# Performance work log

Measured on AMD Instinct MI355X. Metric: run time of the kernel, lower is better.

The kernel has to match this reference:

```python
import jax, jax.numpy as jnp
import numpy as np

DIM = 512
HEADS = 8
WINDOW = 128


def setup_inputs() -> dict:
    key = jax.random.key(0)
    k1, k2, k3, k4 = jax.random.split(key, 4)
    x = jax.random.normal(k1, (16, 4096, DIM), dtype=jnp.float32)
    w_qkv = jax.random.normal(k2, (3 * DIM, DIM), dtype=jnp.float32) * 0.02
    w_proj = jax.random.normal(k3, (DIM, DIM), dtype=jnp.float32) * 0.02
    b_proj = jax.random.normal(k4, (DIM,), dtype=jnp.float32) * 0.02
    return {"x": x, "w_qkv": w_qkv, "w_proj": w_proj, "b_proj": b_proj}


def reference(x, w_qkv, w_proj, b_proj):
    B0, T0, C = x.shape
    H = HEADS
    hd = C // H
    scale = hd ** (-0.5)
    W = WINDOW
    # split into independent windows: [B*T/W, W, C]
    xw = x.reshape(-1, W, C)
    Bw = xw.shape[0]
    # qkv projection (no bias), reshape to [3, Bw, H, W, hd]
    qkv = (xw @ w_qkv.T).reshape(Bw, W, 3, H, hd).transpose(2, 0, 3, 1, 4)
    q, k, v = qkv[0], qkv[1], qkv[2]
    # scaled scores per window: [Bw, H, W, W]
    attn = jnp.einsum("bhqd,bhkd->bhqk", q, k) * scale
    causal_mask = jnp.tril(jnp.ones((W, W), dtype=bool))
    attn = jnp.where(causal_mask, attn, -jnp.inf)
    attn = jax.nn.softmax(attn, axis=-1)
    out = jnp.einsum("bhqk,bhkd->bhqd", attn, v)  # [Bw, H, W, hd]
    out = out.transpose(0, 2, 1, 3).reshape(Bw, W, C)
    out = out @ w_proj.T + b_proj
    return out.reshape(B0, T0, C)
```

## Files before the change

kernel.cpp:

```cpp
#include <hip/hip_runtime.h>
#include <stdint.h>


typedef unsigned short ushort_t;
typedef __attribute__((ext_vector_type(8))) short short8;
typedef __attribute__((ext_vector_type(4))) float f32x4;
typedef __attribute__((ext_vector_type(4))) float f4v;
typedef __attribute__((ext_vector_type(4))) unsigned short us4;

static __device__ __forceinline__ unsigned short f2bf(float f) {
  unsigned int u = __float_as_uint(f);
  u += 0x7FFFu + ((u >> 16) & 1u);
  return (unsigned short)(u >> 16);
}

static __device__ __forceinline__ void gl_lds16(const ushort_t* g, ushort_t* l) {
  __builtin_amdgcn_global_load_lds(
      (const __attribute__((address_space(1))) void*)g,
      (__attribute__((address_space(3))) void*)l, 16, 0, 0);
}

__global__ __launch_bounds__(256) void cast_f32_bf16(const float* __restrict__ in,
                                                     ushort_t* __restrict__ out, int n4) {
  int i = blockIdx.x * 256 + threadIdx.x;
  if (i >= n4) return;
  f4v v = ((const f4v*)in)[i];
  us4 o;
  o.x = f2bf(v.x); o.y = f2bf(v.y); o.z = f2bf(v.z); o.w = f2bf(v.w);
  ((us4*)out)[i] = o;
}

__global__ __launch_bounds__(256) void qkv_gemm(const ushort_t* __restrict__ A,
                                                const ushort_t* __restrict__ B,
                                                ushort_t* __restrict__ qk,
                                                ushort_t* __restrict__ vT) {
  __shared__ __align__(16) ushort_t As[128 * 64];
  __shared__ __align__(16) ushort_t Bs[128 * 64];
  const int tid = threadIdx.x;
  const int lane = tid & 63;
  const int wv = tid >> 6;
  const int wr = wv >> 1, wc = wv & 1;
  const int m0 = blockIdx.x << 7;
  const int n0 = blockIdx.y << 7;
  const int lr = lane & 15;
  const int lg = lane >> 4;
  const int sw = lr & 7;

  f32x4 acc[4][4] = {};

  const int grow = tid >> 3;
  const int gcol = (((tid & 7) ^ (grow & 7)) << 3);
  const ushort_t* gA = A + (size_t)(m0 + grow) * 512 + gcol;
  const ushort_t* gB = B + (size_t)(n0 + grow) * 512 + gcol;

  for (int kk = 0; kk < 512; kk += 64) {
#pragma unroll
    for (int r = 0; r < 4; ++r) {
      gl_lds16(gA + (size_t)(r * 32) * 512 + kk, As + (size_t)(r * 256 + wv * 64) * 8);
      gl_lds16(gB + (size_t)(r * 32) * 512 + kk, Bs + (size_t)(r * 256 + wv * 64) * 8);
    }
    __syncthreads();
#pragma unroll
    for (int ks = 0; ks < 2; ++ks) {
      const int co = ((((ks << 2) | lg) ^ sw) << 3);
      short8 a[4], b[4];
#pragma unroll
      for (int mi = 0; mi < 4; ++mi)
        a[mi] = *(const short8*)(As + (wr * 64 + mi * 16 + lr) * 64 + co);
#pragma unroll
      for (int ni = 0; ni < 4; ++ni)
        b[ni] = *(const short8*)(Bs + (wc * 64 + ni * 16 + lr) * 64 + co);
#pragma unroll
      for (int mi = 0; mi < 4; ++mi)
#pragma unroll
        for (int ni = 0; ni < 4; ++ni)
          acc[mi][ni] = __builtin_amdgcn_mfma_f32_16x16x32_bf16(a[mi], b[ni], acc[mi][ni], 0, 0, 0);
    }
    __syncthreads();
  }

  const int lg4 = lg << 2;
  if (n0 < 1024) {
#pragma unroll
    for (int mi = 0; mi < 4; ++mi) {
      const int rbase = m0 + wr * 64 + mi * 16 + lg4;
#pragma unroll
      for (int ni = 0; ni < 4; ++ni) {
        const int col = n0 + wc * 64 + ni * 16 + lr;
#pragma unroll
        for (int rg = 0; rg < 4; ++rg)
          qk[(size_t)(rbase + rg) * 1024 + col] = f2bf(acc[mi][ni][rg]);
      }
    }
  } else {
    const int win = blockIdx.x;
#pragma unroll
    for (int mi = 0; mi < 4; ++mi) {
      const int t0 = wr * 64 + mi * 16 + lg4;
#pragma unroll
      for (int ni = 0; ni < 4; ++ni) {
        const int c = n0 - 1024 + wc * 64 + ni * 16 + lr;
        const int h = c >> 6, d = c & 63;
        us4 o;
        o.x = f2bf(acc[mi][ni][0]); o.y = f2bf(acc[mi][ni][1]);
        o.z = f2bf(acc[mi][ni][2]); o.w = f2bf(acc[mi][ni][3]);
        *(us4*)(vT + (size_t)((win * 8 + h) * 64 + d) * 128 + t0) = o;
      }
    }
  }
}

__global__ __launch_bounds__(256) void attn_kernel(const ushort_t* __restrict__ qk,
                                                   const ushort_t* __restrict__ vT,
                                                   ushort_t* __restrict__ attn_out) {
  __shared__ __align__(16) ushort_t smem[24576];
  ushort_t* qs = smem;
  ushort_t* ks_ = smem + 8192;
  ushort_t* vs = smem + 16384;
  ushort_t* ps = smem;

  const int tid = threadIdx.x;
  const int lane = tid & 63;
  const int wv = tid >> 6;
  const int win = blockIdx.x >> 3;
  const int h = blockIdx.x & 7;
  const int lr = lane & 15;
  const int lg = lane >> 4;
  const int lg4 = lg << 2;
  const int sw = lr & 7;

  const size_t qbase = (size_t)win * 128 * 1024 + h * 64;
#pragma unroll
  for (int r = 0; r < 4; ++r) {
    const int g = r * 256 + tid;
    const int t = g >> 3, ch = g & 7;
    short8 vq = *(const short8*)(qk + qbase + (size_t)t * 1024 + ch * 8);
    short8 vk = *(const short8*)(qk + qbase + 512 + (size_t)t * 1024 + ch * 8);
    const int st = t * 64 + ((ch ^ (t & 7)) << 3);
    *(short8*)(qs + st) = vq;
    *(short8*)(ks_ + st) = vk;
  }
  const size_t vbase = (size_t)(win * 8 + h) * 64 * 128;
#pragma unroll
  for (int r = 0; r < 4; ++r) {
    const int g = r * 256 + tid;
    const int d = g >> 4, ch = g & 15;
    short8 vvv = *(const short8*)(vT + vbase + (size_t)d * 128 + ch * 8);
    *(short8*)(vs + d * 128 + ((ch ^ (d & 7)) << 3)) = vvv;
  }
  __syncthreads();

  const int rt[2] = {wv, 7 - wv};

  f32x4 sacc[2][8] = {};
#pragma unroll
  for (int ks2 = 0; ks2 < 2; ++ks2) {
    const int co = ((((ks2 << 2) | lg) ^ sw) << 3);
    short8 a0 = *(const short8*)(qs + (rt[0] * 16 + lr) * 64 + co);
    short8 a1 = *(const short8*)(qs + (rt[1] * 16 + lr) * 64 + co);
#pragma unroll
    for (int ni = 0; ni < 8; ++ni) {
      if (ni <= rt[1]) {
        short8 b = *(const short8*)(ks_ + (ni * 16 + lr) * 64 + co);
        if (ni <= rt[0])
          sacc[0][ni] = __builtin_amdgcn_mfma_f32_16x16x32_bf16(a0, b, sacc[0][ni], 0, 0, 0);
        sacc[1][ni] = __builtin_amdgcn_mfma_f32_16x16x32_bf16(a1, b, sacc[1][ni], 0, 0, 0);
      }
    }
  }

  __syncthreads();

  const float C = 0.125f * 1.44269504f;
#pragma unroll
  for (int mi = 0; mi < 2; ++mi) {
    const int r = rt[mi];
    const int rb = r * 16;
#pragma unroll
    for (int ni = 0; ni < 8; ++ni) {
      if (ni <= r) {
#pragma unroll
        for (int rg = 0; rg < 4; ++rg) {
          const int row = rb + lg4 + rg;
          const int col = ni * 16 + lr;
          float e = __builtin_exp2f(sacc[mi][ni][rg] * C);
          e = (col <= row) ? e : 0.0f;
          ps[row * 128 + ((((col >> 3) ^ (row & 7)) << 3) | (col & 7))] = f2bf(e);
        }
      }
    }
    if (!(r & 1)) {
      const int col = (r + 1) * 16 + lr;
#pragma unroll
      for (int rg = 0; rg < 4; ++rg) {
        const int row = rb + lg4 + rg;
        ps[row * 128 + ((((col >> 3) ^ (row & 7)) << 3) | (col & 7))] = 0;
      }
    }
  }

  const short one_bf = (short)0x3F80;
  short8 ones;
#pragma unroll
  for (int j = 0; j < 8; ++j) ones[j] = (lr == 0) ? one_bf : (short)0;

  f32x4 oacc[2][4] = {};
  f32x4 sm[2] = {};
#pragma unroll
  for (int ks2 = 0; ks2 < 4; ++ks2) {
    const int co = ((((ks2 << 2) | lg) ^ sw) << 3);
    if (ks2 <= (rt[1] >> 1)) {
      short8 b[4];
#pragma unroll
      for (int nd = 0; nd < 4; ++nd)
        b[nd] = *(const short8*)(vs + (nd * 16 + lr) * 128 + co);
      short8 a1 = *(const short8*)(ps + (rt[1] * 16 + lr) * 128 + co);
#pragma unroll
      for (int nd = 0; nd < 4; ++nd)
        oacc[1][nd] = __builtin_amdgcn_mfma_f32_16x16x32_bf16(a1, b[nd], oacc[1][nd], 0, 0, 0);
      sm[1] = __builtin_amdgcn_mfma_f32_16x16x32_bf16(a1, ones, sm[1], 0, 0, 0);
      if (ks2 <= (rt[0] >> 1)) {
        short8 a0 = *(const short8*)(ps + (rt[0] * 16 + lr) * 128 + co);
#pragma unroll
        for (int nd = 0; nd < 4; ++nd)
          oacc[0][nd] = __builtin_amdgcn_mfma_f32_16x16x32_bf16(a0, b[nd], oacc[0][nd], 0, 0, 0);
        sm[0] = __builtin_amdgcn_mfma_f32_16x16x32_bf16(a0, ones, sm[0], 0, 0, 0);
      }
    }
  }

  const int src = lane & 48;
  const size_t obase = (size_t)win * 128 * 512 + h * 64;
#pragma unroll
  for (int mi = 0; mi < 2; ++mi) {
    const int rb = rt[mi] * 16;
    float rsv[4];
#pragma unroll
    for (int rg = 0; rg < 4; ++rg)
      rsv[rg] = 1.0f / __shfl(sm[mi][rg], src);
#pragma unroll
    for (int nd = 0; nd < 4; ++nd)
#pragma unroll
      for (int rg = 0; rg < 4; ++rg) {
        const int row = rb + lg4 + rg;
        const int col = nd * 16 + lr;
        attn_out[obase + (size_t)row * 512 + col] = f2bf(oacc[mi][nd][rg] * rsv[rg]);
      }
  }
}

__global__ __launch_bounds__(256) void proj_gemm(const ushort_t* __restrict__ A,
                                                 const ushort_t* __restrict__ B,
                                                 const float* __restrict__ bias,
                                                 float* __restrict__ out) {
  __shared__ __align__(16) ushort_t As[128 * 64];
  __shared__ __align__(16) ushort_t Bs[128 * 64];
  const int tid = threadIdx.x;
  const int lane = tid & 63;
  const int wv = tid >> 6;
  const int wr = wv >> 1, wc = wv & 1;
  const int m0 = blockIdx.x << 7;
  const int n0 = blockIdx.y << 7;
  const int lr = lane & 15;
  const int lg = lane >> 4;
  const int sw = lr & 7;

  f32x4 acc[4][4] = {};

  const int grow = tid >> 3;
  const int gcol = (((tid & 7) ^ (grow & 7)) << 3);
  const ushort_t* gA = A + (size_t)(m0 + grow) * 512 + gcol;
  const ushort_t* gB = B + (size_t)(n0 + grow) * 512 + gcol;

  for (int kk = 0; kk < 512; kk += 64) {
#pragma unroll
    for (int r = 0; r < 4; ++r) {
      gl_lds16(gA + (size_t)(r * 32) * 512 + kk, As + (size_t)(r * 256 + wv * 64) * 8);
      gl_lds16(gB + (size_t)(r * 32) * 512 + kk, Bs + (size_t)(r * 256 + wv * 64) * 8);
    }
    __syncthreads();
#pragma unroll
    for (int ks = 0; ks < 2; ++ks) {
      const int co = ((((ks << 2) | lg) ^ sw) << 3);
      short8 a[4], b[4];
#pragma unroll
      for (int mi = 0; mi < 4; ++mi)
        a[mi] = *(const short8*)(As + (wr * 64 + mi * 16 + lr) * 64 + co);
#pragma unroll
      for (int ni = 0; ni < 4; ++ni)
        b[ni] = *(const short8*)(Bs + (wc * 64 + ni * 16 + lr) * 64 + co);
#pragma unroll
      for (int mi = 0; mi < 4; ++mi)
#pragma unroll
        for (int ni = 0; ni < 4; ++ni)
          acc[mi][ni] = __builtin_amdgcn_mfma_f32_16x16x32_bf16(a[mi], b[ni], acc[mi][ni], 0, 0, 0);
    }
    __syncthreads();
  }

  const int lg4 = lg << 2;
#pragma unroll
  for (int mi = 0; mi < 4; ++mi) {
    const int rbase = m0 + wr * 64 + mi * 16 + lg4;
#pragma unroll
    for (int ni = 0; ni < 4; ++ni) {
      const int col = n0 + wc * 64 + ni * 16 + lr;
      const float bv = bias[col];
#pragma unroll
      for (int rg = 0; rg < 4; ++rg)
        out[(size_t)(rbase + rg) * 512 + col] = acc[mi][ni][rg] + bv;
    }
  }
}

extern "C" void kernel_launch(void* const* d_in, const int* in_sizes, int n_in,
                              void* d_out, int out_size, void* d_ws, size_t ws_size,
                              hipStream_t stream) {
  const float* x      = (const float*)d_in[0];
  const float* w_qkv  = (const float*)d_in[1];
  const float* w_proj = (const float*)d_in[2];
  const float* b_proj = (const float*)d_in[3];
  float* out = (float*)d_out;

  char* ws = (char*)d_ws;
  ushort_t* x_bf     = (ushort_t*)(ws);
  ushort_t* qk_ws    = (ushort_t*)(ws + 67108864);
  ushort_t* vT_ws    = (ushort_t*)(ws + 67108864 + 134217728);
  ushort_t* attn_ws  = (ushort_t*)(ws + 67108864 + 134217728 + 67108864);
  ushort_t* wqkv_bf  = (ushort_t*)(ws + 335544320);
  ushort_t* wproj_bf = (ushort_t*)(ws + 337117184);

  cast_f32_bf16<<<32768, 256, 0, stream>>>(x, x_bf, 8388608);
  cast_f32_bf16<<<768, 256, 0, stream>>>(w_qkv, wqkv_bf, 196608);
  cast_f32_bf16<<<256, 256, 0, stream>>>(w_proj, wproj_bf, 65536);

  qkv_gemm<<<dim3(512, 12), 256, 0, stream>>>(x_bf, wqkv_bf, qk_ws, vT_ws);
  attn_kernel<<<4096, 256, 0, stream>>>(qk_ws, vT_ws, attn_ws);
  proj_gemm<<<dim3(512, 4), 256, 0, stream>>>(attn_ws, wproj_bf, b_proj, out);
}
```

Baseline: 520.2 us.

## Triple-buffer GEMM K-loop with async LDS loads, 256x128 tiles and XCD remap

Result: faster. 477.0 us (-8.3%).

```diff
diff --git a/kernel.cpp b/kernel.cpp
--- a/kernel.cpp
+++ b/kernel.cpp
@@ -30,53 +30,80 @@
   ((us4*)out)[i] = o;
 }
 
-__global__ __launch_bounds__(256) void qkv_gemm(const ushort_t* __restrict__ A,
-                                                const ushort_t* __restrict__ B,
-                                                ushort_t* __restrict__ qk,
-                                                ushort_t* __restrict__ vT) {
-  __shared__ __align__(16) ushort_t As[128 * 64];
-  __shared__ __align__(16) ushort_t Bs[128 * 64];
+__global__ __launch_bounds__(512, 2) void qkv_gemm(const ushort_t* __restrict__ A,
+                                                   const ushort_t* __restrict__ B,
+                                                   ushort_t* __restrict__ qk,
+                                                   ushort_t* __restrict__ vT) {
+  __shared__ __align__(16) ushort_t smem[3 * 24576];
   const int tid = threadIdx.x;
   const int lane = tid & 63;
   const int wv = tid >> 6;
   const int wr = wv >> 1, wc = wv & 1;
-  const int m0 = blockIdx.x << 7;
-  const int n0 = blockIdx.y << 7;
   const int lr = lane & 15;
   const int lg = lane >> 4;
-  const int sw = lr & 7;
+
+  const int bid = blockIdx.x;
+  const int wg = (bid & 7) * 384 + (bid >> 3);
+  const int nb = wg % 12;
+  const int mb = wg / 12;
+  const int m0 = mb << 8;
+  const int n0 = nb << 7;
+
+  const int srow = tid >> 3;
+  const int ssw  = (((tid & 7) ^ (srow & 7)) << 3);
+  const ushort_t* gA = A + (size_t)(m0 + srow) * 512 + ssw;
+  const ushort_t* gB = B + (size_t)(n0 + srow) * 512 + ssw;
 
   f32x4 acc[4][4] = {};
 
-  const int grow = tid >> 3;
-  const int gcol = (((tid & 7) ^ (grow & 7)) << 3);
-  const ushort_t* gA = A + (size_t)(m0 + grow) * 512 + gcol;
-  const ushort_t* gB = B + (size_t)(n0 + grow) * 512 + gcol;
-
-  for (int kk = 0; kk < 512; kk += 64) {
-#pragma unroll
-    for (int r = 0; r < 4; ++r) {
-      gl_lds16(gA + (size_t)(r * 32) * 512 + kk, As + (size_t)(r * 256 + wv * 64) * 8);
-      gl_lds16(gB + (size_t)(r * 32) * 512 + kk, Bs + (size_t)(r * 256 + wv * 64) * 8);
-    }
-    __syncthreads();
+  auto STAGE = [&](int t, int q) {
+    ushort_t* Ab = smem + q * 24576;
+    ushort_t* Bb = Ab + 16384;
+    const int kk = t << 6;
+#pragma unroll
+    for (int r = 0; r < 4; ++r)
+      gl_lds16(gA + (size_t)(r * 64) * 512 + kk, Ab + (r * 512 + wv * 64) * 8);
+#pragma unroll
+    for (int r = 0; r < 2; ++r)
+      gl_lds16(gB + (size_t)(r * 64) * 512 + kk, Bb + (r * 512 + wv * 64) * 8);
+  };
+
+  STAGE(0, 0);
+  STAGE(1, 1);
+  asm volatile("s_waitcnt vmcnt(6)" ::: "memory");
+  __builtin_amdgcn_s_barrier();
+
+#pragma unroll
+  for (int t = 0; t < 8; ++t) {
+    const ushort_t* Ab = smem + (t % 3) * 24576;
+    const ushort_t* Bb = Ab + 16384;
+    short8 a[4][2], b[4][2];
 #pragma unroll
     for (int ks = 0; ks < 2; ++ks) {
-      const int co = ((((ks << 2) | lg) ^ sw) << 3);
-      short8 a[4], b[4];
+      const int co = ((((ks << 2) | lg) ^ (lr & 7)) << 3);
 #pragma unroll
       for (int mi = 0; mi < 4; ++mi)
-        a[mi] = *(const short8*)(As + (wr * 64 + mi * 16 + lr) * 64 + co);
+        a[mi][ks] = *(const short8*)(Ab + (wr * 64 + mi * 16 + lr) * 64 + co);
 #pragma unroll
       for (int ni = 0; ni < 4; ++ni)
-        b[ni] = *(const short8*)(Bs + (wc * 64 + ni * 16 + lr) * 64 + co);
+        b[ni][ks] = *(const short8*)(Bb + (wc * 64 + ni * 16 + lr) * 64 + co);
+    }
+    if (t + 2 < 8) STAGE(t + 2, (t + 2) % 3);
+    if (t < 7) {
+      if (t + 2 < 8) asm volatile("s_waitcnt vmcnt(6)" ::: "memory");
+      else           asm volatile("s_waitcnt vmcnt(0)" ::: "memory");
+      asm volatile("s_waitcnt lgkmcnt(0)" ::: "memory");
+      __builtin_amdgcn_s_barrier();
+    }
+    __builtin_amdgcn_s_setprio(1);
+#pragma unroll
+    for (int ks = 0; ks < 2; ++ks)
 #pragma unroll
       for (int mi = 0; mi < 4; ++mi)
 #pragma unroll
         for (int ni = 0; ni < 4; ++ni)
-          acc[mi][ni] = __builtin_amdgcn_mfma_f32_16x16x32_bf16(a[mi], b[ni], acc[mi][ni], 0, 0, 0);
-    }
-    __syncthreads();
+          acc[mi][ni] = __builtin_amdgcn_mfma_f32_16x16x32_bf16(a[mi][ks], b[ni][ks], acc[mi][ni], 0, 0, 0);
+    __builtin_amdgcn_s_setprio(0);
   }
 
   const int lg4 = lg << 2;
@@ -93,10 +120,11 @@
       }
     }
   } else {
-    const int win = blockIdx.x;
+    const int winb = (m0 >> 7) + (wr >> 1);
+    const int t0b = (wr & 1) * 64;
 #pragma unroll
     for (int mi = 0; mi < 4; ++mi) {
-      const int t0 = wr * 64 + mi * 16 + lg4;
+      const int t0 = t0b + mi * 16 + lg4;
 #pragma unroll
       for (int ni = 0; ni < 4; ++ni) {
         const int c = n0 - 1024 + wc * 64 + ni * 16 + lr;
@@ -104,7 +132,7 @@
         us4 o;
         o.x = f2bf(acc[mi][ni][0]); o.y = f2bf(acc[mi][ni][1]);
         o.z = f2bf(acc[mi][ni][2]); o.w = f2bf(acc[mi][ni][3]);
-        *(us4*)(vT + (size_t)((win * 8 + h) * 64 + d) * 128 + t0) = o;
+        *(us4*)(vT + (size_t)((winb * 8 + h) * 64 + d) * 128 + t0) = o;
       }
     }
   }
@@ -249,53 +277,80 @@
   }
 }
 
-__global__ __launch_bounds__(256) void proj_gemm(const ushort_t* __restrict__ A,
-                                                 const ushort_t* __restrict__ B,
-                                                 const float* __restrict__ bias,
-                                                 float* __restrict__ out) {
-  __shared__ __align__(16) ushort_t As[128 * 64];
-  __shared__ __align__(16) ushort_t Bs[128 * 64];
+__global__ __launch_bounds__(512, 2) void proj_gemm(const ushort_t* __restrict__ A,
+                                                    const ushort_t* __restrict__ B,
+                                                    const float* __restrict__ bias,
+                                                    float* __restrict__ out) {
+  __shared__ __align__(16) ushort_t smem[3 * 24576];
   const int tid = threadIdx.x;
   const int lane = tid & 63;
   const int wv = tid >> 6;
   const int wr = wv >> 1, wc = wv & 1;
-  const int m0 = blockIdx.x << 7;
-  const int n0 = blockIdx.y << 7;
   const int lr = lane & 15;
   const int lg = lane >> 4;
-  const int sw = lr & 7;
+
+  const int bid = blockIdx.x;
+  const int wg = (bid & 7) * 128 + (bid >> 3);
+  const int nb = wg & 3;
+  const int mb = wg >> 2;
+  const int m0 = mb << 8;
+  const int n0 = nb << 7;
+
+  const int srow = tid >> 3;
+  const int ssw  = (((tid & 7) ^ (srow & 7)) << 3);
+  const ushort_t* gA = A + (size_t)(m0 + srow) * 512 + ssw;
+  const ushort_t* gB = B + (size_t)(n0 + srow) * 512 + ssw;
 
   f32x4 acc[4][4] = {};
 
-  const int grow = tid >> 3;
-  const int gcol = (((tid & 7) ^ (grow & 7)) << 3);
-  const ushort_t* gA = A + (size_t)(m0 + grow) * 512 + gcol;
-  const ushort_t* gB = B + (size_t)(n0 + grow) * 512 + gcol;
-
-  for (int kk = 0; kk < 512; kk += 64) {
-#pragma unroll
-    for (int r = 0; r < 4; ++r) {
-      gl_lds16(gA + (size_t)(r * 32) * 512 + kk, As + (size_t)(r * 256 + wv * 64) * 8);
-      gl_lds16(gB + (size_t)(r * 32) * 512 + kk, Bs + (size_t)(r * 256 + wv * 64) * 8);
-    }
-    __syncthreads();
+  auto STAGE = [&](int t, int q) {
+    ushort_t* Ab = smem + q * 24576;
+    ushort_t* Bb = Ab + 16384;
+    const int kk = t << 6;
+#pragma unroll
+    for (int r = 0; r < 4; ++r)
+      gl_lds16(gA + (size_t)(r * 64) * 512 + kk, Ab + (r * 512 + wv * 64) * 8);
+#pragma unroll
+    for (int r = 0; r < 2; ++r)
+      gl_lds16(gB + (size_t)(r * 64) * 512 + kk, Bb + (r * 512 + wv * 64) * 8);
+  };
+
+  STAGE(0, 0);
+  STAGE(1, 1);
+  asm volatile("s_waitcnt vmcnt(6)" ::: "memory");
+  __builtin_amdgcn_s_barrier();
+
+#pragma unroll
+  for (int t = 0; t < 8; ++t) {
+    const ushort_t* Ab = smem + (t % 3) * 24576;
+    const ushort_t* Bb = Ab + 16384;
+    short8 a[4][2], b[4][2];
 #pragma unroll
     for (int ks = 0; ks < 2; ++ks) {
-      const int co = ((((ks << 2) | lg) ^ sw) << 3);
-      short8 a[4], b[4];
+      const int co = ((((ks << 2) | lg) ^ (lr & 7)) << 3);
 #pragma unroll
       for (int mi = 0; mi < 4; ++mi)
-        a[mi] = *(const short8*)(As + (wr * 64 + mi * 16 + lr) * 64 + co);
+        a[mi][ks] = *(const short8*)(Ab + (wr * 64 + mi * 16 + lr) * 64 + co);
 #pragma unroll
       for (int ni = 0; ni < 4; ++ni)
-        b[ni] = *(const short8*)(Bs + (wc * 64 + ni * 16 + lr) * 64 + co);
+        b[ni][ks] = *(const short8*)(Bb + (wc * 64 + ni * 16 + lr) * 64 + co);
+    }
+    if (t + 2 < 8) STAGE(t + 2, (t + 2) % 3);
+    if (t < 7) {
+      if (t + 2 < 8) asm volatile("s_waitcnt vmcnt(6)" ::: "memory");
+      else           asm volatile("s_waitcnt vmcnt(0)" ::: "memory");
+      asm volatile("s_waitcnt lgkmcnt(0)" ::: "memory");
+      __builtin_amdgcn_s_barrier();
+    }
+    __builtin_amdgcn_s_setprio(1);
+#pragma unroll
+    for (int ks = 0; ks < 2; ++ks)
 #pragma unroll
       for (int mi = 0; mi < 4; ++mi)
 #pragma unroll
         for (int ni = 0; ni < 4; ++ni)
-          acc[mi][ni] = __builtin_amdgcn_mfma_f32_16x16x32_bf16(a[mi], b[ni], acc[mi][ni], 0, 0, 0);
-    }
-    __syncthreads();
+          acc[mi][ni] = __builtin_amdgcn_mfma_f32_16x16x32_bf16(a[mi][ks], b[ni][ks], acc[mi][ni], 0, 0, 0);
+    __builtin_amdgcn_s_setprio(0);
   }
 
   const int lg4 = lg << 2;
@@ -334,7 +389,7 @@
   cast_f32_bf16<<<768, 256, 0, stream>>>(w_qkv, wqkv_bf, 196608);
   cast_f32_bf16<<<256, 256, 0, stream>>>(w_proj, wproj_bf, 65536);
 
-  qkv_gemm<<<dim3(512, 12), 256, 0, stream>>>(x_bf, wqkv_bf, qk_ws, vT_ws);
+  qkv_gemm<<<3072, 512, 0, stream>>>(x_bf, wqkv_bf, qk_ws, vT_ws);
   attn_kernel<<<4096, 256, 0, stream>>>(qk_ws, vT_ws, attn_ws);
-  proj_gemm<<<dim3(512, 4), 256, 0, stream>>>(attn_ws, wproj_bf, b_proj, out);
-}
+  proj_gemm<<<1024, 512, 0, stream>>>(attn_ws, wproj_bf, b_proj, out);
+}
```

## Use 256x256 tiles with 4-stage LDS pipeline and XCD-aware block mapping in GEMMs

Applied to the files above, without the earlier changes.

After: 492.1 us. 5.4% less time.

```diff
diff --git a/kernel.cpp b/kernel.cpp
--- a/kernel.cpp
+++ b/kernel.cpp
@@ -30,60 +30,78 @@
   ((us4*)out)[i] = o;
 }
 
-__global__ __launch_bounds__(256) void qkv_gemm(const ushort_t* __restrict__ A,
-                                                const ushort_t* __restrict__ B,
-                                                ushort_t* __restrict__ qk,
-                                                ushort_t* __restrict__ vT) {
-  __shared__ __align__(16) ushort_t As[128 * 64];
-  __shared__ __align__(16) ushort_t Bs[128 * 64];
+__global__ __launch_bounds__(512, 1) void qkv_gemm(const ushort_t* __restrict__ A,
+                                                   const ushort_t* __restrict__ B,
+                                                   ushort_t* __restrict__ qk,
+                                                   ushort_t* __restrict__ vT) {
+  __shared__ __align__(16) ushort_t smem[4 * 16384];
   const int tid = threadIdx.x;
   const int lane = tid & 63;
   const int wv = tid >> 6;
-  const int wr = wv >> 1, wc = wv & 1;
-  const int m0 = blockIdx.x << 7;
-  const int n0 = blockIdx.y << 7;
+  const int wr = wv >> 2;
+  const int wc = wv & 3;
   const int lr = lane & 15;
   const int lg = lane >> 4;
-  const int sw = lr & 7;
-
-  f32x4 acc[4][4] = {};
-
-  const int grow = tid >> 3;
-  const int gcol = (((tid & 7) ^ (grow & 7)) << 3);
-  const ushort_t* gA = A + (size_t)(m0 + grow) * 512 + gcol;
-  const ushort_t* gB = B + (size_t)(n0 + grow) * 512 + gcol;
-
-  for (int kk = 0; kk < 512; kk += 64) {
-#pragma unroll
-    for (int r = 0; r < 4; ++r) {
-      gl_lds16(gA + (size_t)(r * 32) * 512 + kk, As + (size_t)(r * 256 + wv * 64) * 8);
-      gl_lds16(gB + (size_t)(r * 32) * 512 + kk, Bs + (size_t)(r * 256 + wv * 64) * 8);
-    }
-    __syncthreads();
-#pragma unroll
-    for (int ks = 0; ks < 2; ++ks) {
-      const int co = ((((ks << 2) | lg) ^ sw) << 3);
-      short8 a[4], b[4];
-#pragma unroll
-      for (int mi = 0; mi < 4; ++mi)
-        a[mi] = *(const short8*)(As + (wr * 64 + mi * 16 + lr) * 64 + co);
+
+  const int bid = blockIdx.x;
+  const int wg = (bid & 7) * 192 + (bid >> 3);
+  const int nb = wg % 6;
+  const int mb = wg / 6;
+  const int m0 = mb << 8;
+  const int n0 = nb << 8;
+
+  f32x4 acc[8][4] = {};
+  const int co = ((lg ^ ((lr >> 1) & 3)) << 3);
+
+  auto STAGE = [&](int u) {
+    ushort_t* dst = smem + (u & 3) * 16384;
+    const int kk = u << 5;
+#pragma unroll
+    for (int i = 0; i < 2; ++i) {
+      const int g = wv * 128 + i * 64 + lane;
+      const int r = g >> 2;
+      const int ch = (((g & 3) ^ ((r >> 1) & 3)) << 3);
+      gl_lds16(A + (size_t)(m0 + r) * 512 + kk + ch, dst + (wv * 128 + i * 64) * 8);
+      gl_lds16(B + (size_t)(n0 + r) * 512 + kk + ch, dst + 8192 + (wv * 128 + i * 64) * 8);
+    }
+  };
+
+  STAGE(0); STAGE(1); STAGE(2);
+  asm volatile("s_waitcnt vmcnt(8)" ::: "memory");
+  __builtin_amdgcn_s_barrier();
+
+#pragma unroll
+  for (int t = 0; t < 16; ++t) {
+    if (t + 3 < 16) STAGE(t + 3);
+    const ushort_t* Ab = smem + (t & 3) * 16384;
+    const ushort_t* Bb = Ab + 8192;
+    short8 a[8], b[4];
+#pragma unroll
+    for (int mi = 0; mi < 8; ++mi)
+      a[mi] = *(const short8*)(Ab + (wr * 128 + mi * 16 + lr) * 32 + co);
+#pragma unroll
+    for (int ni = 0; ni < 4; ++ni)
+      b[ni] = *(const short8*)(Bb + (wc * 64 + ni * 16 + lr) * 32 + co);
+    __builtin_amdgcn_s_setprio(1);
+#pragma unroll
+    for (int mi = 0; mi < 8; ++mi)
 #pragma unroll
       for (int ni = 0; ni < 4; ++ni)
-        b[ni] = *(const short8*)(Bs + (wc * 64 + ni * 16 + lr) * 64 + co);
-#pragma unroll
-      for (int mi = 0; mi < 4; ++mi)
-#pragma unroll
-        for (int ni = 0; ni < 4; ++ni)
-          acc[mi][ni] = __builtin_amdgcn_mfma_f32_16x16x32_bf16(a[mi], b[ni], acc[mi][ni], 0, 0, 0);
-    }
-    __syncthreads();
+        acc[mi][ni] = __builtin_amdgcn_mfma_f32_16x16x32_bf16(a[mi], b[ni], acc[mi][ni], 0, 0, 0);
+    __builtin_amdgcn_s_setprio(0);
+    if (t < 15) {
+      if (t <= 12)      asm volatile("s_waitcnt vmcnt(8) lgkmcnt(0)" ::: "memory");
+      else if (t == 13) asm volatile("s_waitcnt vmcnt(4) lgkmcnt(0)" ::: "memory");
+      else              asm volatile("s_waitcnt vmcnt(0) lgkmcnt(0)" ::: "memory");
+      __builtin_amdgcn_s_barrier();
+    }
   }
 
   const int lg4 = lg << 2;
   if (n0 < 1024) {
 #pragma unroll
-    for (int mi = 0; mi < 4; ++mi) {
-      const int rbase = m0 + wr * 64 + mi * 16 + lg4;
+    for (int mi = 0; mi < 8; ++mi) {
+      const int rbase = m0 + wr * 128 + mi * 16 + lg4;
 #pragma unroll
       for (int ni = 0; ni < 4; ++ni) {
         const int col = n0 + wc * 64 + ni * 16 + lr;
@@ -93,10 +111,10 @@
       }
     }
   } else {
-    const int win = blockIdx.x;
-#pragma unroll
-    for (int mi = 0; mi < 4; ++mi) {
-      const int t0 = wr * 64 + mi * 16 + lg4;
+    const int winb = (m0 >> 7) + wr;
+#pragma unroll
+    for (int mi = 0; mi < 8; ++mi) {
+      const int t0 = mi * 16 + lg4;
 #pragma unroll
       for (int ni = 0; ni < 4; ++ni) {
         const int c = n0 - 1024 + wc * 64 + ni * 16 + lr;
@@ -104,7 +122,7 @@
         us4 o;
         o.x = f2bf(acc[mi][ni][0]); o.y = f2bf(acc[mi][ni][1]);
         o.z = f2bf(acc[mi][ni][2]); o.w = f2bf(acc[mi][ni][3]);
-        *(us4*)(vT + (size_t)((win * 8 + h) * 64 + d) * 128 + t0) = o;
+        *(us4*)(vT + (size_t)((winb * 8 + h) * 64 + d) * 128 + t0) = o;
       }
     }
   }
@@ -249,59 +267,77 @@
   }
 }
 
-__global__ __launch_bounds__(256) void proj_gemm(const ushort_t* __restrict__ A,
-                                                 const ushort_t* __restrict__ B,
-                                                 const float* __restrict__ bias,
-                                                 float* __restrict__ out) {
-  __shared__ __align__(16) ushort_t As[128 * 64];
-  __shared__ __align__(16) ushort_t Bs[128 * 64];
+__global__ __launch_bounds__(512, 1) void proj_gemm(const ushort_t* __restrict__ A,
+                                                    const ushort_t* __restrict__ B,
+                                                    const float* __restrict__ bias,
+                                                    float* __restrict__ out) {
+  __shared__ __align__(16) ushort_t smem[4 * 16384];
   const int tid = threadIdx.x;
   const int lane = tid & 63;
   const int wv = tid >> 6;
-  const int wr = wv >> 1, wc = wv & 1;
-  const int m0 = blockIdx.x << 7;
-  const int n0 = blockIdx.y << 7;
+  const int wr = wv >> 2;
+  const int wc = wv & 3;
   const int lr = lane & 15;
   const int lg = lane >> 4;
-  const int sw = lr & 7;
-
-  f32x4 acc[4][4] = {};
-
-  const int grow = tid >> 3;
-  const int gcol = (((tid & 7) ^ (grow & 7)) << 3);
-  const ushort_t* gA = A + (size_t)(m0 + grow) * 512 + gcol;
-  const ushort_t* gB = B + (size_t)(n0 + grow) * 512 + gcol;
-
-  for (int kk = 0; kk < 512; kk += 64) {
-#pragma unroll
-    for (int r = 0; r < 4; ++r) {
-      gl_lds16(gA + (size_t)(r * 32) * 512 + kk, As + (size_t)(r * 256 + wv * 64) * 8);
-      gl_lds16(gB + (size_t)(r * 32) * 512 + kk, Bs + (size_t)(r * 256 + wv * 64) * 8);
-    }
-    __syncthreads();
-#pragma unroll
-    for (int ks = 0; ks < 2; ++ks) {
-      const int co = ((((ks << 2) | lg) ^ sw) << 3);
-      short8 a[4], b[4];
-#pragma unroll
-      for (int mi = 0; mi < 4; ++mi)
-        a[mi] = *(const short8*)(As + (wr * 64 + mi * 16 + lr) * 64 + co);
+
+  const int bid = blockIdx.x;
+  const int wg = (bid & 7) * 64 + (bid >> 3);
+  const int nb = wg & 1;
+  const int mb = wg >> 1;
+  const int m0 = mb << 8;
+  const int n0 = nb << 8;
+
+  f32x4 acc[8][4] = {};
+  const int co = ((lg ^ ((lr >> 1) & 3)) << 3);
+
+  auto STAGE = [&](int u) {
+    ushort_t* dst = smem + (u & 3) * 16384;
+    const int kk = u << 5;
+#pragma unroll
+    for (int i = 0; i < 2; ++i) {
+      const int g = wv * 128 + i * 64 + lane;
+      const int r = g >> 2;
+      const int ch = (((g & 3) ^ ((r >> 1) & 3)) << 3);
+      gl_lds16(A + (size_t)(m0 + r) * 512 + kk + ch, dst + (wv * 128 + i * 64) * 8);
+      gl_lds16(B + (size_t)(n0 + r) * 512 + kk + ch, dst + 8192 + (wv * 128 + i * 64) * 8);
+    }
+  };
+
+  STAGE(0); STAGE(1); STAGE(2);
+  asm volatile("s_waitcnt vmcnt(8)" ::: "memory");
+  __builtin_amdgcn_s_barrier();
+
+#pragma unroll
+  for (int t = 0; t < 16; ++t) {
+    if (t + 3 < 16) STAGE(t + 3);
+    const ushort_t* Ab = smem + (t & 3) * 16384;
+    const ushort_t* Bb = Ab + 8192;
+    short8 a[8], b[4];
+#pragma unroll
+    for (int mi = 0; mi < 8; ++mi)
+      a[mi] = *(const short8*)(Ab + (wr * 128 + mi * 16 + lr) * 32 + co);
+#pragma unroll
+    for (int ni = 0; ni < 4; ++ni)
+      b[ni] = *(const short8*)(Bb + (wc * 64 + ni * 16 + lr) * 32 + co);
+    __builtin_amdgcn_s_setprio(1);
+#pragma unroll
+    for (int mi = 0; mi < 8; ++mi)
 #pragma unroll
       for (int ni = 0; ni < 4; ++ni)
-        b[ni] = *(const short8*)(Bs + (wc * 64 + ni * 16 + lr) * 64 + co);
-#pragma unroll
-      for (int mi = 0; mi < 4; ++mi)
-#pragma unroll
-        for (int ni = 0; ni < 4; ++ni)
-          acc[mi][ni] = __builtin_amdgcn_mfma_f32_16x16x32_bf16(a[mi], b[ni], acc[mi][ni], 0, 0, 0);
-    }
-    __syncthreads();
+        acc[mi][ni] = __builtin_amdgcn_mfma_f32_16x16x32_bf16(a[mi], b[ni], acc[mi][ni], 0, 0, 0);
+    __builtin_amdgcn_s_setprio(0);
+    if (t < 15) {
+      if (t <= 12)      asm volatile("s_waitcnt vmcnt(8) lgkmcnt(0)" ::: "memory");
+      else if (t == 13) asm volatile("s_waitcnt vmcnt(4) lgkmcnt(0)" ::: "memory");
+      else              asm volatile("s_waitcnt vmcnt(0) lgkmcnt(0)" ::: "memory");
+      __builtin_amdgcn_s_barrier();
+    }
   }
 
   const int lg4 = lg << 2;
 #pragma unroll
-  for (int mi = 0; mi < 4; ++mi) {
-    const int rbase = m0 + wr * 64 + mi * 16 + lg4;
+  for (int mi = 0; mi < 8; ++mi) {
+    const int rbase = m0 + wr * 128 + mi * 16 + lg4;
 #pragma unroll
     for (int ni = 0; ni < 4; ++ni) {
       const int col = n0 + wc * 64 + ni * 16 + lr;
@@ -334,7 +370,7 @@
   cast_f32_bf16<<<768, 256, 0, stream>>>(w_qkv, wqkv_bf, 196608);
   cast_f32_bf16<<<256, 256, 0, stream>>>(w_proj, wproj_bf, 65536);
 
-  qkv_gemm<<<dim3(512, 12), 256, 0, stream>>>(x_bf, wqkv_bf, qk_ws, vT_ws);
+  qkv_gemm<<<1536, 512, 0, stream>>>(x_bf, wqkv_bf, qk_ws, vT_ws);
   attn_kernel<<<4096, 256, 0, stream>>>(qk_ws, vT_ws, attn_ws);
-  proj_gemm<<<dim3(512, 4), 256, 0, stream>>>(attn_ws, wproj_bf, b_proj, out);
-}
+  proj_gemm<<<512, 512, 0, stream>>>(attn_ws, wproj_bf, b_proj, out);
+}
```
